# Kernel tuning notes

Measured on AMD Instinct MI355X. Metric: run time of the kernel, lower is better.

The kernel has to match this reference:

```python
import jax, jax.numpy as jnp
import numpy as np
from jax import lax

B, C, H, W = 4, 1024, 25, 25
CH = [1, 10, 10, 1]  # NeighConsensus channels
K = 3                # 4D kernel size (3,3,3,3)


def setup_inputs() -> dict:
    key = jax.random.key(0)
    ks = jax.random.split(key, 8)
    inp = {
        "feature_A": jax.random.normal(ks[0], (B, C, H, W), jnp.float32),
        "feature_B": jax.random.normal(ks[1], (B, C, H, W), jnp.float32),
    }
    for i in range(3):
        cin, cout = CH[i], CH[i + 1]
        scale = 1.0 / np.sqrt(cin * K ** 4)
        inp[f"W{i+1}"] = jax.random.normal(ks[2 + 2 * i], (cout, cin, K, K, K, K), jnp.float32) * scale
        inp[f"b{i+1}"] = jnp.zeros((cout,), jnp.float32)
    return inp


def feature_l2norm(x, axis=1):
    # torch: x / sqrt(sum(x^2, dim)+1e-6)
    return x / jnp.sqrt(jnp.sum(x * x, axis=axis, keepdims=True) + 1e-6)


# 4D convolution: lhs [B,C,f1,f2,f3,f4], rhs [Cout,Cin,k,k,k,k]
_DN = lax.ConvDimensionNumbers(lhs_spec=(0, 1, 2, 3, 4, 5),
                               rhs_spec=(0, 1, 2, 3, 4, 5),
                               out_spec=(0, 1, 2, 3, 4, 5))


def conv4d(x, w, b):
    p = K // 2
    y = lax.conv_general_dilated(x, w, (1, 1, 1, 1), [(p, p)] * 4, dimension_numbers=_DN)
    return y + b[None, :, None, None, None, None]


def nc_stack(x, Ws, bs):
    # Conv4d + ReLU stack (CreateCon4D)
    for w, b in zip(Ws, bs):
        x = jax.nn.relu(conv4d(x, w, b))
    return x


def neigh_consensus(x, Ws, bs):
    # symmetric_mode: conv(x) + permuted conv of the (AB)->(BA) swapped tensor
    perm = (0, 1, 4, 5, 2, 3)
    return nc_stack(x, Ws, bs) + jnp.transpose(nc_stack(jnp.transpose(x, perm), Ws, bs), perm)


def mutual_matching(corr):
    # corr: [B,1,f1,f2,f3,f4]
    eps = 1e-5
    max_B = jnp.max(corr, axis=(2, 3), keepdims=True)  # max over (f1,f2)
    max_A = jnp.max(corr, axis=(4, 5), keepdims=True)  # max over (f3,f4)
    return corr * (corr / (max_A + eps)) * (corr / (max_B + eps))


def correlation(fA, fB):
    # FeatureCorrelation with normalization=True
    corr = jnp.einsum('bchw,bcij->bhwij', fA, fB)[:, None]  # [B,1,hA,wA,hB,wB]
    corr = jax.nn.relu(corr)
    # featureL2Norm over the singleton channel dim == elementwise x/sqrt(x^2+eps)
    return corr / jnp.sqrt(corr * corr + 1e-6)


def reference(feature_A, feature_B, W1, b1, W2, b2, W3, b3):
    fA = feature_l2norm(feature_A)
    fB = feature_l2norm(feature_B)
    corr4d = correlation(fA, fB)
    corr4d = mutual_matching(corr4d)
    corr4d = neigh_consensus(corr4d, (W1, W2, W3), (b1, b2, b3))
    corr4d = mutual_matching(corr4d)
    return corr4d
```

## Files before the change

### kernel.cpp

```cpp
#include <hip/hip_runtime.h>
#include <math.h>

#define HWQ 625
#define NPOSQ 390625
#define NB 4
#define NCH 1024

typedef __attribute__((ext_vector_type(8))) short bf16x8;
typedef __attribute__((ext_vector_type(4))) float f32x4;

__device__ inline unsigned short f2bf(float x) {
    union { float f; unsigned int u; } c; c.f = x;
    unsigned int u = c.u;
    return (unsigned short)((u + 0x7fffu + ((u >> 16) & 1u)) >> 16);
}

__global__ void pack_misc_kernel(const float* __restrict__ W1, const float* __restrict__ b1,
                                 const float* __restrict__ b2,
                                 float* __restrict__ W1P, float* __restrict__ bL1,
                                 float* __restrict__ bL2)
{
    int t = blockIdx.x * blockDim.x + threadIdx.x;
    if (t < 1620) {
        int co = t % 20; int r = t / 20; int e = r / 9, t34 = r % 9;
        W1P[t] = (co < 10) ? W1[co * 81 + e * 9 + t34] : W1[(co - 10) * 81 + t34 * 9 + e];
    }
    if (t < 20) { bL1[t] = b1[t % 10]; bL2[t] = b2[t % 10]; }
}

__global__ void pack_mfma_w2_kernel(const float* __restrict__ W2,
                                    unsigned short* __restrict__ Ablob)
{
    int t = blockIdx.x * blockDim.x + threadIdx.x;
    if (t >= 54 * 64) return;
    int frag = t >> 6, lane = t & 63;
    int g = frag / 27; int r1 = frag % 27; int kstep = r1 / 9; int dd = r1 % 9;
    int d3 = dd / 3, d4 = dd % 3;
    int co = lane & 15;
    unsigned short v[8];
#pragma unroll
    for (int j = 0; j < 8; ++j) {
        int k = kstep * 32 + ((lane >> 4) << 3) + j;
        float w = 0.0f;
        if (co < 10 && k < 90) {
            int ci = k / 9, e = k % 9, d1 = e / 3, d2 = e % 3;
            int tap = (g == 0) ? (d1 * 27 + d2 * 9 + d3 * 3 + d4)
                               : (d3 * 27 + d4 * 9 + d1 * 3 + d2);
            w = W2[(co * 10 + ci) * 81 + tap];
        }
        v[j] = f2bf(w);
    }
    uint4 val;
    val.x = (unsigned)v[0] | ((unsigned)v[1] << 16);
    val.y = (unsigned)v[2] | ((unsigned)v[3] << 16);
    val.z = (unsigned)v[4] | ((unsigned)v[5] << 16);
    val.w = (unsigned)v[6] | ((unsigned)v[7] << 16);
    *(uint4*)(Ablob + (size_t)frag * 512 + lane * 8) = val;
}

__global__ void pack_mfma_w3_kernel(const float* __restrict__ W3,
                                    unsigned short* __restrict__ Ablob3)
{
    int t = blockIdx.x * blockDim.x + threadIdx.x;
    if (t >= 54 * 64) return;
    int frag = t >> 6, lane = t & 63;
    int kstep = frag / 9, dd = frag % 9;
    int d3 = dd / 3, d4 = dd % 3;
    int row = lane & 15;
    unsigned short v[8];
#pragma unroll
    for (int j = 0; j < 8; ++j) {
        int k = kstep * 32 + ((lane >> 4) << 3) + j;
        float w = 0.0f;
        if (k < 180) {
            int g = k / 90, rem = k - g * 90;
            int ci = rem / 9, e = rem % 9;
            if (row == g) {
                int d1 = e / 3, d2 = e % 3;
                int tap = (g == 0) ? (d1 * 27 + d2 * 9 + d3 * 3 + d4)
                                   : (d3 * 27 + d4 * 9 + d1 * 3 + d2);
                w = W3[ci * 81 + tap];
            }
        }
        v[j] = f2bf(w);
    }
    uint4 val;
    val.x = (unsigned)v[0] | ((unsigned)v[1] << 16);
    val.y = (unsigned)v[2] | ((unsigned)v[3] << 16);
    val.z = (unsigned)v[4] | ((unsigned)v[5] << 16);
    val.w = (unsigned)v[6] | ((unsigned)v[7] << 16);
    *(uint4*)(Ablob3 + (size_t)frag * 512 + lane * 8) = val;
}

__global__ void invnorm_kernel(const float* __restrict__ fA, const float* __restrict__ fB,
                               float* __restrict__ invA, float* __restrict__ invB)
{
    int idx = blockIdx.x * blockDim.x + threadIdx.x;
    if (idx >= NB * HWQ) return;
    const float* f = blockIdx.y ? fB : fA;
    float* o = blockIdx.y ? invB : invA;
    int b = idx / HWQ, m = idx - b * HWQ;
    const float* p = f + (size_t)b * NCH * HWQ + m;
    float s = 0.f;
    for (int c = 0; c < NCH; c += 4) {
        float x0 = p[(c + 0) * HWQ], x1 = p[(c + 1) * HWQ];
        float x2 = p[(c + 2) * HWQ], x3 = p[(c + 3) * HWQ];
        s += x0 * x0 + x1 * x1 + x2 * x2 + x3 * x3;
    }
    o[idx] = 1.0f / sqrtf(s + 1e-6f);
}

__global__ __launch_bounds__(256) void corr_gemm_kernel(
    const float* __restrict__ fA, const float* __restrict__ fB,
    const float* __restrict__ invA, const float* __restrict__ invB,
    float* __restrict__ corr)
{
    __shared__ float As[16][64];
    __shared__ float Bs[16][64];
    const int b = blockIdx.z;
    const int m0 = blockIdx.y * 64, n0 = blockIdx.x * 64;
    const int tid = threadIdx.x;
    const int tx = tid & 15, ty = tid >> 4;
    float acc[4][4] = {};
    const float* Ab = fA + (size_t)b * NCH * HWQ;
    const float* Bb = fB + (size_t)b * NCH * HWQ;
    for (int k0 = 0; k0 < NCH; k0 += 16) {
        for (int i = tid; i < 1024; i += 256) {
            int k = i >> 6, mm = i & 63;
            int gm = m0 + mm, gn = n0 + mm;
            As[k][mm] = (gm < HWQ) ? Ab[(k0 + k) * HWQ + gm] : 0.0f;
            Bs[k][mm] = (gn < HWQ) ? Bb[(k0 + k) * HWQ + gn] : 0.0f;
        }
        __syncthreads();
#pragma unroll
        for (int k = 0; k < 16; ++k) {
            float4 a4 = *(const float4*)&As[k][ty * 4];
            float4 b4 = *(const float4*)&Bs[k][tx * 4];
            float av[4] = {a4.x, a4.y, a4.z, a4.w};
            float bv[4] = {b4.x, b4.y, b4.z, b4.w};
#pragma unroll
            for (int i = 0; i < 4; ++i)
#pragma unroll
                for (int j = 0; j < 4; ++j)
                    acc[i][j] = fmaf(av[i], bv[j], acc[i][j]);
        }
        __syncthreads();
    }
#pragma unroll
    for (int i = 0; i < 4; ++i) {
        int m = m0 + ty * 4 + i;
        if (m >= HWQ) continue;
        float ia = invA[b * HWQ + m];
#pragma unroll
        for (int j = 0; j < 4; ++j) {
            int n = n0 + tx * 4 + j;
            if (n >= HWQ) continue;
            float v = acc[i][j] * ia * invB[b * HWQ + n];
            v = fmaxf(v, 0.0f);
            v = v / sqrtf(v * v + 1e-6f);
            corr[((size_t)b * HWQ + m) * HWQ + n] = v;
        }
    }
}

__global__ void rowmax_kernel(const float* __restrict__ s, float* __restrict__ rmax)
{
    int row = blockIdx.x * 4 + (threadIdx.x >> 6);
    int lane = threadIdx.x & 63;
    if (row >= NB * HWQ) return;
    const float* p = s + (size_t)row * HWQ;
    float v = -1e30f;
    for (int n = lane; n < HWQ; n += 64) v = fmaxf(v, p[n]);
    for (int off = 32; off; off >>= 1) v = fmaxf(v, __shfl_xor(v, off));
    if (lane == 0) rmax[row] = v;
}

__global__ void colmax_kernel(const float* __restrict__ s, float* __restrict__ cmax)
{
    int b = blockIdx.x;
    int col = blockIdx.y * 128 + threadIdx.x;
    if (col >= HWQ) return;
    const float* p = s + (size_t)b * NPOSQ + col;
    float v = -1e30f;
    for (int m = 0; m < HWQ; ++m) v = fmaxf(v, p[m * HWQ]);
    cmax[b * HWQ + col] = v;
}

__global__ void mm_apply_kernel(const float* __restrict__ s, const float* __restrict__ rmax,
                                const float* __restrict__ cmax, float* __restrict__ out)
{
    int idx = blockIdx.x * blockDim.x + threadIdx.x;
    if (idx >= NB * NPOSQ) return;
    int b = idx / NPOSQ, rem = idx - b * NPOSQ;
    int m = rem / HWQ, n = rem - m * HWQ;
    float v = s[idx];
    out[idx] = v * v * v / ((rmax[b * HWQ + m] + 1e-5f) * (cmax[b * HWQ + n] + 1e-5f));
}

__global__ __launch_bounds__(192) void conv4d_l1(
    const float* __restrict__ corr, const float* __restrict__ W1P,
    const float* __restrict__ bL1, unsigned short* __restrict__ x1)
{
    __shared__ float sp[9 * 784];
    __shared__ float wl[1620];
    const int f12 = blockIdx.x;
    const float* in = corr + (size_t)blockIdx.z * NPOSQ;
    unsigned short* out = x1 + (size_t)blockIdx.z * 20 * NPOSQ;
    const int f1 = f12 / 25, f2 = f12 - f1 * 25;
    const int tid = threadIdx.x;

    for (int i = tid; i < 9 * 784; i += 192) sp[i] = 0.0f;
    for (int i = tid; i < 1620; i += 192) wl[i] = W1P[i];

    const int tt = (tid < 169) ? tid : 0;
    const int ty = tt / 13, tx = tt - ty * 13;
    const int r0 = ty * 2, c0 = tx * 2;

    float acc[20][4];
#pragma unroll
    for (int co = 0; co < 20; ++co) {
        float bv = bL1[co];
        acc[co][0] = bv; acc[co][1] = bv; acc[co][2] = bv; acc[co][3] = bv;
    }

    __syncthreads();
    for (int i = tid; i < 5625; i += 192) {
        int e = i / 625, q = i - e * 625;
        int d1 = e / 3, d2 = e - d1 * 3;
        int f1n = f1 + d1 - 1, f2n = f2 + d2 - 1;
        float v = 0.0f;
        if (((unsigned)f1n < 25u) & ((unsigned)f2n < 25u))
            v = in[(f1n * 25 + f2n) * HWQ + q];
        int rr = q / 25, cc = q - rr * 25;
        sp[e * 784 + (rr + 1) * 28 + (cc + 1)] = v;
    }
    __syncthreads();

#pragma unroll 1
    for (int e = 0; e < 9; ++e) {
        float win[16];
        const int base = e * 784 + r0 * 28 + c0;
#pragma unroll
        for (int a = 0; a < 4; ++a)
#pragma unroll
            for (int bb = 0; bb < 4; ++bb)
                win[a * 4 + bb] = sp[base + a * 28 + bb];
#pragma unroll
        for (int t34 = 0; t34 < 9; ++t34) {
            int d3 = t34 / 3, d4 = t34 - d3 * 3;
            float x0 = win[d3 * 4 + d4], x1v = win[d3 * 4 + d4 + 1];
            float x2v = win[(d3 + 1) * 4 + d4], x3v = win[(d3 + 1) * 4 + d4 + 1];
            const float* wp = wl + (e * 9 + t34) * 20;
#pragma unroll
            for (int c4 = 0; c4 < 5; ++c4) {
                float4 w4 = *(const float4*)(wp + c4 * 4);
                float wv[4] = {w4.x, w4.y, w4.z, w4.w};
#pragma unroll
                for (int q4 = 0; q4 < 4; ++q4) {
                    int co = c4 * 4 + q4;
                    acc[co][0] = fmaf(x0, wv[q4], acc[co][0]);
                    acc[co][1] = fmaf(x1v, wv[q4], acc[co][1]);
                    acc[co][2] = fmaf(x2v, wv[q4], acc[co][2]);
                    acc[co][3] = fmaf(x3v, wv[q4], acc[co][3]);
                }
            }
        }
    }

    if (tid < 169) {
#pragma unroll
        for (int co = 0; co < 20; ++co) {
            unsigned short* op = out + (size_t)co * NPOSQ + f12 * 625;
#pragma unroll
            for (int i = 0; i < 2; ++i)
#pragma unroll
                for (int j = 0; j < 2; ++j) {
                    int f3 = r0 + i, f4 = c0 + j;
                    if (f3 < 25 && f4 < 25)
                        op[f3 * 25 + f4] = f2bf(fmaxf(acc[co][i * 2 + j], 0.0f));
                }
        }
    }
}

#define L2S 36
#define L2ROWS 736

#define STAGE_PRE()                                                         \
    int qoff_[6]; unsigned dsto_[6]; unsigned inqm = 0;                     \
    _Pragma("unroll")                                                       \
    for (int it = 0; it < 6; ++it) {                                        \
        int task = tid + it * 512;                                          \
        int qp = task >> 2;                                                 \
        int u = qp / 27, v = qp - u * 27;                                   \
        int f3i = u - 1, f4i = v - 1;                                       \
        bool inq = (task < 2916) & ((unsigned)f3i < 25u) & ((unsigned)f4i < 25u); \
        if (inq) inqm |= (1u << it);                                        \
        qoff_[it] = f3i * 25 + f4i;                                         \
        dsto_[it] = (task < 2916) ? (unsigned)(qp * L2S + kg * 8) : 0u;     \
    }                                                                       \
    unsigned bpo_[7];                                                       \
    _Pragma("unroll")                                                       \
    for (int j = 0; j < 7; ++j) {                                           \
        int t = wave + j * 8;                                               \
        int f3 = t >> 1, h = t & 1;                                         \
        bpo_[j] = (unsigned)(((f3 * 27 + h * 16 + lo16) * L2S + kqg) * 2);  \
    }

#define STAGE_KSTEP(INPTR)                                                  \
    _Pragma("unroll")                                                       \
    for (int it = 0; it < 6; ++it) {                                        \
        if (tid + it * 512 < 2916) {                                        \
            bool inq = (inqm >> it) & 1;                                    \
            int qoff = qoff_[it];                                           \
            unsigned short vals[8];                                         \
            _Pragma("unroll")                                               \
            for (int j = 0; j < 8; ++j)                                     \
                vals[j] = (inq && ((vmask >> j) & 1)) ? (INPTR)[poff[j] + qoff] \
                                                      : (unsigned short)0;  \
            unsigned short* dst = sp + dsto_[it];                           \
            uint2 w0, w1;                                                   \
            w0.x = (unsigned)vals[0] | ((unsigned)vals[1] << 16);           \
            w0.y = (unsigned)vals[2] | ((unsigned)vals[3] << 16);           \
            w1.x = (unsigned)vals[4] | ((unsigned)vals[5] << 16);           \
            w1.y = (unsigned)vals[6] | ((unsigned)vals[7] << 16);           \
            *(uint2*)dst = w0;                                              \
            *(uint2*)(dst + 4) = w1;                                        \
        }                                                                   \
    }

#define MFMA_KSTEP(ABASE)                                                   \
    {                                                                       \
        bf16x8 afA = *(const bf16x8*)(ABASE);                               \
        _Pragma("unroll")                                                   \
        for (int dd = 0; dd < 9; ++dd) {                                    \
            bf16x8 afN = (dd < 8) ? *(const bf16x8*)((ABASE) + (dd + 1) * 512) : afA; \
            const int d3 = dd / 3, d4 = dd - d3 * 3;                        \
            const int imm = (d3 * 27 + d4) * (L2S * 2);                     \
            _Pragma("unroll")                                               \
            for (int j = 0; j < 7; ++j) {                                   \
                if (j < 6 || wave < 2) {                                    \
                    const char* rp = (const char*)sp + (bpo_[j] + imm);     \
                    uint2 p0 = *(const uint2*)rp;                           \
                    uint2 p1 = *(const uint2*)(rp + 8);                     \
                    union { unsigned u[4]; bf16x8 v; } cv;                  \
                    cv.u[0] = p0.x; cv.u[1] = p0.y; cv.u[2] = p1.x; cv.u[3] = p1.y; \
                    acc[j] = __builtin_amdgcn_mfma_f32_16x16x32_bf16(afA, cv.v, acc[j], 0, 0, 0); \
                }                                                           \
            }                                                               \
            afA = afN;                                                      \
        }                                                                   \
    }

__global__ __launch_bounds__(512) void conv4d_mfma_l2(
    const unsigned short* __restrict__ x1, const unsigned short* __restrict__ Ablob,
    const float* __restrict__ bL2, unsigned short* __restrict__ x2)
{
    __shared__ alignas(16) unsigned short sp[L2ROWS * L2S];
    const int f12 = blockIdx.x, g = blockIdx.y;
    const unsigned short* in = x1 + (size_t)blockIdx.z * 20 * NPOSQ;
    unsigned short* out = x2 + (size_t)blockIdx.z * 20 * NPOSQ;
    const int f1 = f12 / 25, f2 = f12 - f1 * 25;
    const int tid = threadIdx.x, wave = tid >> 6, lane = tid & 63;
    const int lo16 = lane & 15, kqg = (lane >> 4) << 3;
    const int kg = tid & 3;

    f32x4 acc[7];
#pragma unroll
    for (int j = 0; j < 7; ++j) acc[j] = (f32x4){0.f, 0.f, 0.f, 0.f};
    const unsigned short* Ag = Ablob + (size_t)g * 27 * 512;

    STAGE_PRE();

#pragma unroll 1
    for (int kstep = 0; kstep < 3; ++kstep) {
        unsigned poff[8];
        unsigned vmask = 0;
        const int kbase = kstep * 32 + kg * 8;
#pragma unroll
        for (int j = 0; j < 8; ++j) {
            int cie = kbase + j;
            int ci = cie / 9, e = cie - ci * 9;
            int f1n = f1 + e / 3 - 1, f2n = f2 + e % 3 - 1;
            if ((cie < 90) & ((unsigned)f1n < 25u) & ((unsigned)f2n < 25u)) vmask |= (1u << j);
            poff[j] = (unsigned)((g * 10 + ci) * NPOSQ + (f1n * 25 + f2n) * 625);
        }
        __syncthreads();
        STAGE_KSTEP(in);
        __syncthreads();
        const unsigned short* Abase = Ag + (size_t)(kstep * 9) * 512 + lane * 8;
        MFMA_KSTEP(Abase);
    }

    int t = wave;
    for (int j = 0; j < 7; ++j, t += 8) {
        if (t < 50) {
            int f3 = t >> 1, h = t & 1;
            int f4 = h * 16 + lo16;
            if (f4 < 25) {
#pragma unroll
                for (int r = 0; r < 4; ++r) {
                    int co = (lane >> 4) * 4 + r;
                    if (co < 10) {
                        float v = acc[j][r] + bL2[g * 10 + co];
                        out[(size_t)(g * 10 + co) * NPOSQ + f12 * 625 + f3 * 25 + f4] =
                            f2bf(fmaxf(v, 0.0f));
                    }
                }
            }
        }
    }
}

__global__ __launch_bounds__(512) void conv4d_mfma_l3(
    const unsigned short* __restrict__ x2, const unsigned short* __restrict__ Ablob3,
    const float* __restrict__ b3p, float* __restrict__ sbuf)
{
    __shared__ alignas(16) unsigned short sp[L2ROWS * L2S];
    const int f12 = blockIdx.x;
    const unsigned short* in = x2 + (size_t)blockIdx.z * 20 * NPOSQ;
    float* out = sbuf + (size_t)blockIdx.z * NPOSQ;
    const int f1 = f12 / 25, f2 = f12 - f1 * 25;
    const int tid = threadIdx.x, wave = tid >> 6, lane = tid & 63;
    const int lo16 = lane & 15, kqg = (lane >> 4) << 3;
    const int kg = tid & 3;

    f32x4 acc[7];
#pragma unroll
    for (int j = 0; j < 7; ++j) acc[j] = (f32x4){0.f, 0.f, 0.f, 0.f};

    STAGE_PRE();

#pragma unroll 1
    for (int kstep = 0; kstep < 6; ++kstep) {
        unsigned poff[8];
        unsigned vmask = 0;
        const int kbase = kstep * 32 + kg * 8;
#pragma unroll
        for (int j = 0; j < 8; ++j) {
            int cie = kbase + j;
            int plane = cie / 9, e = cie - plane * 9;
            int f1n = f1 + e / 3 - 1, f2n = f2 + e % 3 - 1;
            if ((cie < 180) & ((unsigned)f1n < 25u) & ((unsigned)f2n < 25u)) vmask |= (1u << j);
            poff[j] = (unsigned)(plane * NPOSQ + (f1n * 25 + f2n) * 625);
        }
        __syncthreads();
        STAGE_KSTEP(in);
        __syncthreads();
        const unsigned short* Abase = Ablob3 + (size_t)(kstep * 9) * 512 + lane * 8;
        MFMA_KSTEP(Abase);
    }

    const float b3v = b3p[0];
    if ((lane >> 4) == 0) {
        int t = wave;
        for (int j = 0; j < 7; ++j, t += 8) {
            if (t < 50) {
                int f3 = t >> 1, h = t & 1;
                int f4 = h * 16 + lo16;
                if (f4 < 25) {
                    float s0 = fmaxf(acc[j][0] + b3v, 0.0f);
                    float s1 = fmaxf(acc[j][1] + b3v, 0.0f);
                    out[f12 * 625 + f3 * 25 + f4] = s0 + s1;
                }
            }
        }
    }
}

extern "C" void kernel_launch(void* const* d_in, const int* in_sizes, int n_in,
                              void* d_out, int out_size, void* d_ws, size_t ws_size,
                              hipStream_t stream)
{
    const float* fA = (const float*)d_in[0];
    const float* fB = (const float*)d_in[1];
    const float* W1 = (const float*)d_in[2];
    const float* b1 = (const float*)d_in[3];
    const float* W2 = (const float*)d_in[4];
    const float* b2 = (const float*)d_in[5];
    const float* W3 = (const float*)d_in[6];
    const float* b3 = (const float*)d_in[7];
    float* out = (float*)d_out;
    float* ws = (float*)d_ws;

    float* invA = ws + 0;
    float* invB = ws + 2500;
    float* rmax = ws + 5000;
    float* cmax = ws + 7500;
    float* W1P  = ws + 10000;
    float* bL1  = ws + 11620;
    float* bL2  = ws + 11640;
    unsigned short* Ablob2 = (unsigned short*)(ws + 12000);
    unsigned short* Ablob3 = (unsigned short*)(ws + 25824);
    float* corr = ws + 40000;
    float* sbuf = ws + 1602500;
    unsigned short* x1b = (unsigned short*)(ws + 3165000);

    const size_t REQ = (size_t)34415000 * 4;
    const bool fused = ws_size >= REQ;
    unsigned short* x2b = fused ? (unsigned short*)(ws + 18790000)
                                : (unsigned short*)(ws + 7080000);

    hipLaunchKernelGGL(pack_misc_kernel, dim3(7), dim3(256), 0, stream, W1, b1, b2, W1P, bL1, bL2);
    hipLaunchKernelGGL(pack_mfma_w2_kernel, dim3(14), dim3(256), 0, stream, W2, Ablob2);
    hipLaunchKernelGGL(pack_mfma_w3_kernel, dim3(14), dim3(256), 0, stream, W3, Ablob3);
    hipLaunchKernelGGL(invnorm_kernel, dim3(10, 2), dim3(256), 0, stream, fA, fB, invA, invB);
    hipLaunchKernelGGL(corr_gemm_kernel, dim3(10, 10, 4), dim3(256), 0, stream,
                       fA, fB, invA, invB, corr);
    hipLaunchKernelGGL(rowmax_kernel, dim3(625), dim3(256), 0, stream, corr, rmax);
    hipLaunchKernelGGL(colmax_kernel, dim3(4, 5), dim3(128), 0, stream, corr, cmax);
    hipLaunchKernelGGL(mm_apply_kernel, dim3(6104), dim3(256), 0, stream, corr, rmax, cmax, corr);

    if (fused) {
        hipLaunchKernelGGL(conv4d_l1, dim3(625, 1, NB), dim3(192), 0, stream, corr, W1P, bL1, x1b);
        hipLaunchKernelGGL(conv4d_mfma_l2, dim3(625, 2, NB), dim3(512), 0, stream,
                           x1b, Ablob2, bL2, x2b);
        hipLaunchKernelGGL(conv4d_mfma_l3, dim3(625, 1, NB), dim3(512), 0, stream,
                           x2b, Ablob3, b3, sbuf);
    } else {
        for (int b = 0; b < NB; ++b) {
            hipLaunchKernelGGL(conv4d_l1, dim3(625, 1, 1), dim3(192), 0, stream,
                               corr + (size_t)b * NPOSQ, W1P, bL1, x1b);
            hipLaunchKernelGGL(conv4d_mfma_l2, dim3(625, 2, 1), dim3(512), 0, stream,
                               x1b, Ablob2, bL2, x2b);
            hipLaunchKernelGGL(conv4d_mfma_l3, dim3(625, 1, 1), dim3(512), 0, stream,
                               x2b, Ablob3, b3, sbuf + (size_t)b * NPOSQ);
        }
    }

    hipLaunchKernelGGL(rowmax_kernel, dim3(625), dim3(256), 0, stream, sbuf, rmax);
    hipLaunchKernelGGL(colmax_kernel, dim3(4, 5), dim3(128), 0, stream, sbuf, cmax);
    hipLaunchKernelGGL(mm_apply_kernel, dim3(6104), dim3(256), 0, stream, sbuf, rmax, cmax, out);
}
```

Before: 1.081 ms.

## Store intermediate activations position-major and stage planes with coalesced lane-contiguous loads

Intermediate activation tensors change layout from channel-major ([ch][f12][625]) to position-major ([f12][ch][625]), so the 625-element plane for each (neighbour position, channel) sits contiguously near the others. Staging into shared memory now has each wave handle four K-slices and each lane load consecutive elements of a plane, which gives coalesced global reads in place of the earlier scattered 8-way gathers. The halo is zeroed once up front rather than rewritten every step. In exchange, each lane writes 2-byte scalars to LDS, which may cause bank conflicts, and the extra zeroing pass adds some startup cost.

Result: slower. 1.265 ms (+17.0%).

```diff
diff --git a/kernel.cpp b/kernel.cpp
--- a/kernel.cpp
+++ b/kernel.cpp
@@ -268,9 +268,10 @@
     }
 
     if (tid < 169) {
+        unsigned short* ob = out + (size_t)f12 * 20 * 625;
 #pragma unroll
         for (int co = 0; co < 20; ++co) {
-            unsigned short* op = out + (size_t)co * NPOSQ + f12 * 625;
+            unsigned short* op = ob + co * 625;
 #pragma unroll
             for (int i = 0; i < 2; ++i)
 #pragma unroll
@@ -287,17 +288,12 @@
 #define L2ROWS 736
 
 #define STAGE_PRE()                                                         \
-    int qoff_[6]; unsigned dsto_[6]; unsigned inqm = 0;                     \
+    int dstw_[10];                                                          \
     _Pragma("unroll")                                                       \
-    for (int it = 0; it < 6; ++it) {                                        \
-        int task = tid + it * 512;                                          \
-        int qp = task >> 2;                                                 \
-        int u = qp / 27, v = qp - u * 27;                                   \
-        int f3i = u - 1, f4i = v - 1;                                       \
-        bool inq = (task < 2916) & ((unsigned)f3i < 25u) & ((unsigned)f4i < 25u); \
-        if (inq) inqm |= (1u << it);                                        \
-        qoff_[it] = f3i * 25 + f4i;                                         \
-        dsto_[it] = (task < 2916) ? (unsigned)(qp * L2S + kg * 8) : 0u;     \
+    for (int pass = 0; pass < 10; ++pass) {                                 \
+        int idx = pass * 64 + lane;                                         \
+        int rr = idx / 25, cc = idx - rr * 25;                              \
+        dstw_[pass] = ((rr + 1) * 27 + cc + 1) * (L2S * 2) + wave * 8;      \
     }                                                                       \
     unsigned bpo_[7];                                                       \
     _Pragma("unroll")                                                       \
@@ -307,25 +303,21 @@
         bpo_[j] = (unsigned)(((f3 * 27 + h * 16 + lo16) * L2S + kqg) * 2);  \
     }
 
-#define STAGE_KSTEP(INPTR)                                                  \
+#define STAGE_KSTEP(INPTR, CHOFF, CIE_MAX)                                  \
     _Pragma("unroll")                                                       \
-    for (int it = 0; it < 6; ++it) {                                        \
-        if (tid + it * 512 < 2916) {                                        \
-            bool inq = (inqm >> it) & 1;                                    \
-            int qoff = qoff_[it];                                           \
-            unsigned short vals[8];                                         \
-            _Pragma("unroll")                                               \
-            for (int j = 0; j < 8; ++j)                                     \
-                vals[j] = (inq && ((vmask >> j) & 1)) ? (INPTR)[poff[j] + qoff] \
-                                                      : (unsigned short)0;  \
-            unsigned short* dst = sp + dsto_[it];                           \
-            uint2 w0, w1;                                                   \
-            w0.x = (unsigned)vals[0] | ((unsigned)vals[1] << 16);           \
-            w0.y = (unsigned)vals[2] | ((unsigned)vals[3] << 16);           \
-            w1.x = (unsigned)vals[4] | ((unsigned)vals[5] << 16);           \
-            w1.y = (unsigned)vals[6] | ((unsigned)vals[7] << 16);           \
-            *(uint2*)dst = w0;                                              \
-            *(uint2*)(dst + 4) = w1;                                        \
+    for (int i = 0; i < 4; ++i) {                                           \
+        int cie = ksbase + wave * 4 + i;                                    \
+        int ci = cie / 9, e = cie - ci * 9;                                 \
+        int f1n = f1 + e / 3 - 1, f2n = f2 + (e - (e / 3) * 3) - 1;         \
+        bool valid = (cie < (CIE_MAX)) & ((unsigned)f1n < 25u) & ((unsigned)f2n < 25u); \
+        int pidx = valid ? ((f1n * 25 + f2n) * 20 + (CHOFF) + ci) : 0;      \
+        const unsigned short* gp = (INPTR) + (size_t)pidx * 625;            \
+        _Pragma("unroll")                                                   \
+        for (int pass = 0; pass < 10; ++pass) {                             \
+            if (pass < 9 || lane < 49) {                                    \
+                unsigned short v = valid ? gp[pass * 64 + lane] : (unsigned short)0; \
+                *(unsigned short*)((char*)sp + (dstw_[pass] + i * 2)) = v;  \
+            }                                                               \
         }                                                                   \
     }
 
@@ -363,7 +355,8 @@
     const int f1 = f12 / 25, f2 = f12 - f1 * 25;
     const int tid = threadIdx.x, wave = tid >> 6, lane = tid & 63;
     const int lo16 = lane & 15, kqg = (lane >> 4) << 3;
-    const int kg = tid & 3;
+
+    for (int i = tid; i < L2ROWS * L2S / 2; i += 512) ((unsigned*)sp)[i] = 0u;
 
     f32x4 acc[7];
 #pragma unroll
@@ -374,24 +367,15 @@
 
 #pragma unroll 1
     for (int kstep = 0; kstep < 3; ++kstep) {
-        unsigned poff[8];
-        unsigned vmask = 0;
-        const int kbase = kstep * 32 + kg * 8;
-#pragma unroll
-        for (int j = 0; j < 8; ++j) {
-            int cie = kbase + j;
-            int ci = cie / 9, e = cie - ci * 9;
-            int f1n = f1 + e / 3 - 1, f2n = f2 + e % 3 - 1;
-            if ((cie < 90) & ((unsigned)f1n < 25u) & ((unsigned)f2n < 25u)) vmask |= (1u << j);
-            poff[j] = (unsigned)((g * 10 + ci) * NPOSQ + (f1n * 25 + f2n) * 625);
-        }
+        const int ksbase = kstep * 32;
         __syncthreads();
-        STAGE_KSTEP(in);
+        STAGE_KSTEP(in, g * 10, 90);
         __syncthreads();
         const unsigned short* Abase = Ag + (size_t)(kstep * 9) * 512 + lane * 8;
         MFMA_KSTEP(Abase);
     }
 
+    unsigned short* ob = out + (size_t)f12 * 20 * 625 + g * 10 * 625;
     int t = wave;
     for (int j = 0; j < 7; ++j, t += 8) {
         if (t < 50) {
@@ -403,8 +387,7 @@
                     int co = (lane >> 4) * 4 + r;
                     if (co < 10) {
                         float v = acc[j][r] + bL2[g * 10 + co];
-                        out[(size_t)(g * 10 + co) * NPOSQ + f12 * 625 + f3 * 25 + f4] =
-                            f2bf(fmaxf(v, 0.0f));
+                        ob[co * 625 + f3 * 25 + f4] = f2bf(fmaxf(v, 0.0f));
                     }
                 }
             }
@@ -423,7 +406,8 @@
     const int f1 = f12 / 25, f2 = f12 - f1 * 25;
     const int tid = threadIdx.x, wave = tid >> 6, lane = tid & 63;
     const int lo16 = lane & 15, kqg = (lane >> 4) << 3;
-    const int kg = tid & 3;
+
+    for (int i = tid; i < L2ROWS * L2S / 2; i += 512) ((unsigned*)sp)[i] = 0u;
 
     f32x4 acc[7];
 #pragma unroll
@@ -433,19 +417,9 @@
 
 #pragma unroll 1
     for (int kstep = 0; kstep < 6; ++kstep) {
-        unsigned poff[8];
-        unsigned vmask = 0;
-        const int kbase = kstep * 32 + kg * 8;
-#pragma unroll
-        for (int j = 0; j < 8; ++j) {
-            int cie = kbase + j;
-            int plane = cie / 9, e = cie - plane * 9;
-            int f1n = f1 + e / 3 - 1, f2n = f2 + e % 3 - 1;
-            if ((cie < 180) & ((unsigned)f1n < 25u) & ((unsigned)f2n < 25u)) vmask |= (1u << j);
-            poff[j] = (unsigned)(plane * NPOSQ + (f1n * 25 + f2n) * 625);
-        }
+        const int ksbase = kstep * 32;
         __syncthreads();
-        STAGE_KSTEP(in);
+        STAGE_KSTEP(in, 0, 180);
         __syncthreads();
         const unsigned short* Abase = Ablob3 + (size_t)(kstep * 9) * 512 + lane * 8;
         MFMA_KSTEP(Abase);
```
